# Optimization experiments

Measured on AMD Instinct MI355X. Metric: run time of the kernel, lower is better.

## Reference

```python
import jax, jax.numpy as jnp
from jax import lax
import numpy as np

DIM = 256
QK = 256          # qk_dim defaults to dim
HEADS = 8
NWIN = 7
TOPK = 4
KS = 3            # side_dwconv


def setup_inputs() -> dict:
    key = jax.random.key(0)
    ks = jax.random.split(key, 8)
    B, H, W = 1, 112, 112
    s = lambda d: 1.0 / np.sqrt(d)
    return {
        "x": jax.random.normal(ks[0], (B, H, W, DIM), jnp.float32),
        # fused qkv linear: dim -> qk + qk + dim
        "w_qkv": jax.random.normal(ks[1], (DIM, 2 * QK + DIM), jnp.float32) * s(DIM),
        "b_qkv": jnp.zeros((2 * QK + DIM,), jnp.float32),
        # output projection
        "w_o": jax.random.normal(ks[2], (DIM, DIM), jnp.float32) * s(DIM),
        "b_o": jnp.zeros((DIM,), jnp.float32),
        # depthwise 3x3 lepe conv (HWIO with I=1, groups=dim)
        "lepe_w": jax.random.normal(ks[3], (KS, KS, 1, DIM), jnp.float32) * s(KS * KS),
        "lepe_b": jnp.zeros((DIM,), jnp.float32),
    }


def _win2img(t, B, H, W, c):
    # (B, p2, h, w, c) windows -> (B, H, W, c) image
    hw, ww = H // NWIN, W // NWIN
    t = t.reshape(B, NWIN, NWIN, hw, ww, c)
    return t.transpose(0, 1, 3, 2, 4, 5).reshape(B, H, W, c)


def reference(x, w_qkv, b_qkv, w_o, b_o, lepe_w, lepe_b):
    B, H, W, C = x.shape
    hw, ww = H // NWIN, W // NWIN
    p2, w2 = NWIN * NWIN, hw * ww
    hd_q, hd_v = QK // HEADS, DIM // HEADS
    scale = QK ** (-0.5)

    # partition into windows: (B, p2, hw, ww, C)
    xp = x.reshape(B, NWIN, hw, NWIN, ww, C).transpose(0, 1, 3, 2, 4, 5)
    xp = xp.reshape(B, p2, hw, ww, C)

    qkv = xp @ w_qkv + b_qkv
    q, kv = qkv[..., :QK], qkv[..., QK:]          # (B,p2,hw,ww,QK), (...,QK+DIM)

    q_pix = q.reshape(B, p2, w2, QK)
    kv_pix = kv.reshape(B, p2, w2, QK + DIM)      # identity kv_down

    # region-level routing (detached in original since diff_routing=False)
    q_win = lax.stop_gradient(q.mean((2, 3)))     # (B,p2,QK)
    k_win = lax.stop_gradient(kv[..., :QK].mean((2, 3)))
    logit = (q_win * scale) @ jnp.swapaxes(k_win, -1, -2)   # (B,p2,p2)
    top_logit, top_idx = lax.top_k(logit, TOPK)             # (B,p2,TOPK)
    r_weight = jax.nn.softmax(top_logit, axis=-1)           # unused: mul_weight='none'

    # gather top-k regions' KV: (B, p2, TOPK, w2, QK+DIM)
    kv_sel = jax.vmap(lambda kvb, idxb: kvb[idxb])(kv_pix, top_idx)

    k_sel = kv_sel[..., :QK].reshape(B, p2, TOPK * w2, HEADS, hd_q)
    v_sel = kv_sel[..., QK:].reshape(B, p2, TOPK * w2, HEADS, hd_v)
    qh = q_pix.reshape(B, p2, w2, HEADS, hd_q)

    attn = jnp.einsum('bpqhc,bpkhc->bphqk', qh * scale, k_sel)
    attn = jax.nn.softmax(attn, axis=-1)
    out = jnp.einsum('bphqk,bpkhc->bpqhc', attn, v_sel).reshape(B, p2, hw, ww, DIM)
    out = _win2img(out, B, H, W, DIM)

    # lepe: depthwise conv over v in image layout
    v_img = _win2img(kv[..., QK:], B, H, W, DIM)
    lepe = lax.conv_general_dilated(
        v_img, lepe_w, (1, 1), 'SAME',
        dimension_numbers=('NHWC', 'HWIO', 'NHWC'),
        feature_group_count=DIM) + lepe_b

    return (out + lepe) @ w_o + b_o
```

## Files before the change

### kernel.cpp

```cpp
#include <hip/hip_runtime.h>
#include <math.h>


typedef __bf16 bf16x8 __attribute__((ext_vector_type(8)));
typedef __bf16 bf16x4 __attribute__((ext_vector_type(4)));
typedef float f32x4 __attribute__((ext_vector_type(4)));

__global__ __launch_bounds__(64)
void pack1(const float* __restrict__ w_qkv, const float* __restrict__ w_o,
           __bf16* __restrict__ wtq, __bf16* __restrict__ wto,
           float* __restrict__ qkwin) {
    const int b = blockIdx.x;
    const int t = threadIdx.x;
    if (b < 768) {
        int n = b;
        int k = t * 4;
        bf16x4 o;
        o[0] = (__bf16)w_qkv[(k + 0) * 768 + n];
        o[1] = (__bf16)w_qkv[(k + 1) * 768 + n];
        o[2] = (__bf16)w_qkv[(k + 2) * 768 + n];
        o[3] = (__bf16)w_qkv[(k + 3) * 768 + n];
        *(bf16x4*)(wtq + (size_t)n * 256 + k) = o;
    } else if (b < 1024) {
        int n = b - 768;
        int k = t * 4;
        bf16x4 o;
        o[0] = (__bf16)w_o[(k + 0) * 256 + n];
        o[1] = (__bf16)w_o[(k + 1) * 256 + n];
        o[2] = (__bf16)w_o[(k + 2) * 256 + n];
        o[3] = (__bf16)w_o[(k + 3) * 256 + n];
        *(bf16x4*)(wto + (size_t)n * 256 + k) = o;
    } else {
        int idx = (b - 1024) * 64 + t;
        *(float4*)(qkwin + (size_t)idx * 4) = (float4){0.f, 0.f, 0.f, 0.f};
    }
}

template<int QKV>
__global__ __launch_bounds__(256)
void gemm_bf16(const __bf16* __restrict__ A,
               const float* __restrict__ Ax,
               const __bf16* __restrict__ Wt,
               const float* __restrict__ bias,
               float* __restrict__ C, int N,
               __bf16* __restrict__ Qp,
               __bf16* __restrict__ Kp,
               __bf16* __restrict__ vbf,
               __bf16* __restrict__ Vt,
               float* __restrict__ q_win,
               float* __restrict__ k_win) {
    const int t = threadIdx.x & 63;
    const int wv = threadIdx.x >> 6;
    const int l16 = t & 15, quad = t >> 4;
    const int m0 = blockIdx.x * 64;
    const int n0 = blockIdx.y * 128 + wv * 32;

    __shared__ __bf16 Vs[128][72];

    int mrow[4];
#pragma unroll
    for (int nt = 0; nt < 4; nt++) {
        const int m = m0 + nt * 16 + l16;
        if (QKV == 1) {
            const int p = m >> 8, pix = m & 255;
            mrow[nt] = ((p / 7) * 16 + (pix >> 4)) * 112 + (p % 7) * 16 + (pix & 15);
        } else {
            mrow[nt] = m;
        }
    }

    f32x4 acc[2][4];
#pragma unroll
    for (int km = 0; km < 2; km++)
#pragma unroll
        for (int nt = 0; nt < 4; nt++) acc[km][nt] = (f32x4){0.f, 0.f, 0.f, 0.f};

#pragma unroll
    for (int ks = 0; ks < 8; ks++) {
        bf16x8 Af[2], Bf[4];
#pragma unroll
        for (int km = 0; km < 2; km++)
            Af[km] = *(const bf16x8*)(Wt + (size_t)(n0 + km * 16 + l16) * 256 + ks * 32 + quad * 8);
#pragma unroll
        for (int nt = 0; nt < 4; nt++) {
            if (QKV == 1) {
                const float* s = Ax + (size_t)mrow[nt] * 256 + ks * 32 + quad * 8;
                const float4 f0 = *(const float4*)s;
                const float4 f1 = *(const float4*)(s + 4);
                bf16x8 bv;
                bv[0] = (__bf16)f0.x; bv[1] = (__bf16)f0.y;
                bv[2] = (__bf16)f0.z; bv[3] = (__bf16)f0.w;
                bv[4] = (__bf16)f1.x; bv[5] = (__bf16)f1.y;
                bv[6] = (__bf16)f1.z; bv[7] = (__bf16)f1.w;
                Bf[nt] = bv;
            } else {
                Bf[nt] = *(const bf16x8*)(A + (size_t)mrow[nt] * 256 + ks * 32 + quad * 8);
            }
        }
#pragma unroll
        for (int km = 0; km < 2; km++)
#pragma unroll
            for (int nt = 0; nt < 4; nt++)
                acc[km][nt] = __builtin_amdgcn_mfma_f32_16x16x32_bf16(
                    Af[km], Bf[nt], acc[km][nt], 0, 0, 0);
    }

    float ws[2][4];
#pragma unroll
    for (int km = 0; km < 2; km++)
#pragma unroll
        for (int j = 0; j < 4; j++) ws[km][j] = 0.f;

#pragma unroll
    for (int km = 0; km < 2; km++) {
        const int n = n0 + km * 16 + quad * 4;
        float4 b4 = *(const float4*)(bias + n);
#pragma unroll
        for (int nt = 0; nt < 4; nt++) {
            const int m = m0 + nt * 16 + l16;
            float v0 = acc[km][nt][0] + b4.x;
            float v1 = acc[km][nt][1] + b4.y;
            float v2 = acc[km][nt][2] + b4.z;
            float v3 = acc[km][nt][3] + b4.w;
            if (QKV == 0) {
                float4 o = {v0, v1, v2, v3};
                *(float4*)(C + (size_t)m * N + n) = o;
            } else {
                const int p = m >> 8, pix = m & 255;
                if (n0 < 512) {
                    ws[km][0] += v0; ws[km][1] += v1;
                    ws[km][2] += v2; ws[km][3] += v3;
                }
                if (n0 < 256) {
                    const float s = 1.4426950408889634f / 16.0f;
                    int h = n >> 5, cc = n & 31;
                    bf16x4 o;
                    o[0] = (__bf16)(v0 * s); o[1] = (__bf16)(v1 * s);
                    o[2] = (__bf16)(v2 * s); o[3] = (__bf16)(v3 * s);
                    *(bf16x4*)(Qp + ((size_t)((p * 8 + h) * 256 + pix)) * 32 + cc) = o;
                } else if (n0 < 512) {
                    int n2 = n - 256;
                    int h = n2 >> 5, cc = n2 & 31;
                    bf16x4 o;
                    o[0] = (__bf16)v0; o[1] = (__bf16)v1;
                    o[2] = (__bf16)v2; o[3] = (__bf16)v3;
                    *(bf16x4*)(Kp + ((size_t)((p * 8 + h) * 256 + pix)) * 32 + cc) = o;
                } else {
                    int n2 = n - 512;
                    int imgrow = ((p / 7) * 16 + (pix >> 4)) * 112 + (p % 7) * 16 + (pix & 15);
                    bf16x4 o;
                    o[0] = (__bf16)v0; o[1] = (__bf16)v1;
                    o[2] = (__bf16)v2; o[3] = (__bf16)v3;
                    *(bf16x4*)(vbf + (size_t)imgrow * 256 + n2) = o;
                    const int cbase = wv * 32 + km * 16 + quad * 4;
                    const int pb = nt * 16 + l16;
                    Vs[cbase + 0][pb] = o[0];
                    Vs[cbase + 1][pb] = o[1];
                    Vs[cbase + 2][pb] = o[2];
                    Vs[cbase + 3][pb] = o[3];
                }
            }
        }
    }

    if (QKV == 1 && n0 < 512) {
        const int pblk = m0 >> 8;
#pragma unroll
        for (int km = 0; km < 2; km++) {
#pragma unroll
            for (int j = 0; j < 4; j++) {
                float s = ws[km][j];
                s += __shfl_xor(s, 1);
                s += __shfl_xor(s, 2);
                s += __shfl_xor(s, 4);
                s += __shfl_xor(s, 8);
                ws[km][j] = s;
            }
            if (l16 == 0) {
                const int n = n0 + km * 16 + quad * 4;
                float* dst = (n < 256) ? (q_win + pblk * 256 + n)
                                       : (k_win + pblk * 256 + (n - 256));
                atomicAdd(dst + 0, ws[km][0]);
                atomicAdd(dst + 1, ws[km][1]);
                atomicAdd(dst + 2, ws[km][2]);
                atomicAdd(dst + 3, ws[km][3]);
            }
        }
    }

    if (QKV == 1 && blockIdx.y >= 4) {
        __syncthreads();
        const int p_ = m0 >> 8, qt_ = (m0 >> 6) & 3;
        const int vb = blockIdx.y * 128 - 512;
#pragma unroll
        for (int rep = 0; rep < 4; rep++) {
            int id = rep * 256 + threadIdx.x;
            int row = id >> 3, c8 = (id & 7) * 8;
            int hh = (vb + row) >> 5, c32 = (vb + row) & 31;
            bf16x8 val = *(const bf16x8*)&Vs[row][c8];
            *(bf16x8*)(Vt + ((size_t)((p_ * 8 + hh) * 32 + c32)) * 256 + qt_ * 64 + c8) = val;
        }
    }
}

__global__ __launch_bounds__(64)
void routing_topk(const float* __restrict__ q_win,
                  const float* __restrict__ k_win,
                  int* __restrict__ top_idx) {
    const int r = blockIdx.x;
    const int j = threadIdx.x;
    __shared__ float vals[64];

    float d = -1e30f;
    if (j < 49) {
        const float4* qp = (const float4*)(q_win + r * 256);
        const float4* kp = (const float4*)(k_win + j * 256);
        float s = 0.f;
#pragma unroll
        for (int c = 0; c < 64; c++) {
            float4 a = qp[c], b = kp[c];
            s += a.x * b.x + a.y * b.y + a.z * b.z + a.w * b.w;
        }
        d = s;
    }
    vals[j] = d;
    __syncthreads();
    if (j == 0) {
        float bv0 = -1e30f, bv1 = -1e30f, bv2 = -1e30f, bv3 = -1e30f;
        int bi0 = 0, bi1 = 0, bi2 = 0, bi3 = 0;
        for (int q = 0; q < 49; q++) {
            float v = vals[q];
            if (v > bv0) {
                bv3 = bv2; bi3 = bi2; bv2 = bv1; bi2 = bi1; bv1 = bv0; bi1 = bi0;
                bv0 = v; bi0 = q;
            } else if (v > bv1) {
                bv3 = bv2; bi3 = bi2; bv2 = bv1; bi2 = bi1; bv1 = v; bi1 = q;
            } else if (v > bv2) {
                bv3 = bv2; bi3 = bi2; bv2 = v; bi2 = q;
            } else if (v > bv3) {
                bv3 = v; bi3 = q;
            }
        }
        top_idx[r * 4 + 0] = bi0;
        top_idx[r * 4 + 1] = bi1;
        top_idx[r * 4 + 2] = bi2;
        top_idx[r * 4 + 3] = bi3;
    }
}

#define PLDS_PITCH 68
#define HALO_PITCH 36

__global__ __launch_bounds__(256)
void attn_mfma(const __bf16* __restrict__ Qp,
               const __bf16* __restrict__ Kp,
               const __bf16* __restrict__ Vt,
               const int* __restrict__ top_idx,
               const __bf16* __restrict__ vbf,
               const float* __restrict__ lw,
               const float* __restrict__ lb,
               __bf16* __restrict__ prebf) {
    const int bb = blockIdx.x;
    const int qt = bb / 392;
    const int ph = bb - qt * 392;
    const int p = ph >> 3;
    const int h = ph & 7;
    const int t = threadIdx.x & 63;
    const int wv = threadIdx.x >> 6;
    const int l16 = t & 15, quad = t >> 4;

    __shared__ union {
        unsigned short Plds[4][64 * PLDS_PITCH];
        struct {
            f32x4 O[4][2][4][64];
            float l[4][4][64];
        } red;
    } U;
    __shared__ __bf16 Hs[108 * HALO_PITCH];

    unsigned short* const Pw = U.Plds[wv];

    bf16x8 Qf[4];
#pragma unroll
    for (int nt = 0; nt < 4; nt++)
        Qf[nt] = *(const bf16x8*)(Qp + ((size_t)((p * 8 + h) * 256 + qt * 64 + nt * 16 + l16)) * 32 + quad * 8);

    const int sel = top_idx[p * 4 + wv];
    const __bf16* const Kb = Kp + ((size_t)(sel * 8 + h)) * 8192;
    const __bf16* const Vb = Vt + ((size_t)(sel * 8 + h)) * 8192;

    float lstate[4] = {0.f, 0.f, 0.f, 0.f};
    f32x4 O[2][4];
#pragma unroll
    for (int mt = 0; mt < 2; mt++)
#pragma unroll
        for (int nt = 0; nt < 4; nt++) O[mt][nt] = (f32x4){0.f, 0.f, 0.f, 0.f};

    bf16x8 Kf[4];
#pragma unroll
    for (int km = 0; km < 4; km++)
        Kf[km] = *(const bf16x8*)(Kb + (size_t)(km * 16 + l16) * 32 + quad * 8);

    for (int kc = 0; kc < 4; kc++) {
        const int kbase = kc * 64;

        bf16x8 Vf[2][2];
#pragma unroll
        for (int ks = 0; ks < 2; ks++)
#pragma unroll
            for (int mt = 0; mt < 2; mt++)
                Vf[ks][mt] = *(const bf16x8*)(Vb + (size_t)(mt * 16 + l16) * 256 + kbase + ks * 32 + quad * 8);

        const int kbn = (kc < 3 ? kc + 1 : 3) * 64;
        bf16x8 Kn[4];
#pragma unroll
        for (int km = 0; km < 4; km++)
            Kn[km] = *(const bf16x8*)(Kb + (size_t)(kbn + km * 16 + l16) * 32 + quad * 8);

#pragma unroll
        for (int nt = 0; nt < 4; nt++) {
            f32x4 S[4];
            __builtin_amdgcn_s_setprio(1);
#pragma unroll
            for (int km = 0; km < 4; km++)
                S[km] = __builtin_amdgcn_mfma_f32_16x16x32_bf16(
                    Kf[km], Qf[nt], (f32x4){0.f, 0.f, 0.f, 0.f}, 0, 0, 0);
            __builtin_amdgcn_s_setprio(0);

            float rs = 0.f;
#pragma unroll
            for (int km = 0; km < 4; km++) {
                union { unsigned short u[4]; ushort4 v; } pk;
#pragma unroll
                for (int r = 0; r < 4; r++) {
                    float pv = __builtin_amdgcn_exp2f(S[km][r]);
                    rs += pv;
                    pk.u[r] = __builtin_bit_cast(unsigned short, (__bf16)pv);
                }
                *(ushort4*)&Pw[(nt * 16 + l16) * PLDS_PITCH + km * 16 + quad * 4] = pk.v;
            }
            rs += __shfl_xor(rs, 16);
            rs += __shfl_xor(rs, 32);
            lstate[nt] += rs;
        }

#pragma unroll
        for (int ks = 0; ks < 2; ks++) {
#pragma unroll
            for (int nt = 0; nt < 4; nt++) {
                int idx = (nt * 16 + l16) * PLDS_PITCH + ks * 32 + quad * 8;
                union { ushort4 u4[2]; bf16x8 v; } pu;
                pu.u4[0] = *(const ushort4*)&Pw[idx];
                pu.u4[1] = *(const ushort4*)&Pw[idx + 4];
                __builtin_amdgcn_s_setprio(1);
#pragma unroll
                for (int mt = 0; mt < 2; mt++)
                    O[mt][nt] = __builtin_amdgcn_mfma_f32_16x16x32_bf16(
                        Vf[ks][mt], pu.v, O[mt][nt], 0, 0, 0);
                __builtin_amdgcn_s_setprio(0);
            }
        }

#pragma unroll
        for (int km = 0; km < 4; km++) Kf[km] = Kn[km];
    }

    __syncthreads();
#pragma unroll
    for (int mt = 0; mt < 2; mt++)
#pragma unroll
        for (int nt = 0; nt < 4; nt++)
            U.red.O[wv][mt][nt][t] = O[mt][nt];
#pragma unroll
    for (int nt = 0; nt < 4; nt++)
        U.red.l[wv][nt][t] = lstate[nt];

    const int pr = p / 7, pc = p % 7;
    if (threadIdx.x < 108) {
        const int i = threadIdx.x;
        int hy = i / 18, hx = i - hy * 18;
        int gy = pr * 16 + qt * 4 - 1 + hy;
        int gx = pc * 16 - 1 + hx;
        union { bf16x4 v4[8]; bf16x8 v8[4]; uint4 q[4]; } u;
        u.q[0] = (uint4){0u, 0u, 0u, 0u};
        u.q[1] = (uint4){0u, 0u, 0u, 0u};
        u.q[2] = (uint4){0u, 0u, 0u, 0u};
        u.q[3] = (uint4){0u, 0u, 0u, 0u};
        if (gy >= 0 && gy < 112 && gx >= 0 && gx < 112) {
            const __bf16* src = vbf + ((size_t)(gy * 112 + gx)) * 256 + h * 32;
            u.v8[0] = *(const bf16x8*)src;
            u.v8[1] = *(const bf16x8*)(src + 8);
            u.v8[2] = *(const bf16x8*)(src + 16);
            u.v8[3] = *(const bf16x8*)(src + 24);
        }
#pragma unroll
        for (int j = 0; j < 8; j++)
            *(bf16x4*)&Hs[i * HALO_PITCH + j * 4] = u.v4[j];
    }
    __syncthreads();

    const int nt = wv;
    const float ltot = U.red.l[0][nt][t] + U.red.l[1][nt][t]
                     + U.red.l[2][nt][t] + U.red.l[3][nt][t];
    const float inv = 1.f / ltot;
    const int himg = pr * 16 + qt * 4 + nt, wimg = pc * 16 + l16;
#pragma unroll
    for (int mt = 0; mt < 2; mt++) {
        f32x4 o = U.red.O[0][mt][nt][t];
#pragma unroll
        for (int v = 1; v < 4; v++) {
            f32x4 ov = U.red.O[v][mt][nt][t];
            o[0] += ov[0]; o[1] += ov[1]; o[2] += ov[2]; o[3] += ov[3];
        }
        const int c = h * 32 + mt * 16 + quad * 4;
        const float4 lbv = *(const float4*)(lb + c);
        float a0 = lbv.x, a1 = lbv.y, a2 = lbv.z, a3 = lbv.w;
#pragma unroll
        for (int dh = 0; dh < 3; dh++)
#pragma unroll
            for (int dw = 0; dw < 3; dw++) {
                const float4 w4 = *(const float4*)(lw + (dh * 3 + dw) * 256 + c);
                const bf16x4 v4 = *(const bf16x4*)&Hs[((nt + dh) * 18 + l16 + dw) * HALO_PITCH + mt * 16 + quad * 4];
                a0 += (float)v4[0] * w4.x;
                a1 += (float)v4[1] * w4.y;
                a2 += (float)v4[2] * w4.z;
                a3 += (float)v4[3] * w4.w;
            }
        bf16x4 ob;
        ob[0] = (__bf16)(o[0] * inv + a0);
        ob[1] = (__bf16)(o[1] * inv + a1);
        ob[2] = (__bf16)(o[2] * inv + a2);
        ob[3] = (__bf16)(o[3] * inv + a3);
        *(bf16x4*)(prebf + ((size_t)(himg * 112 + wimg)) * 256 + c) = ob;
    }
}

extern "C" void kernel_launch(void* const* d_in, const int* in_sizes, int n_in,
                              void* d_out, int out_size, void* d_ws, size_t ws_size,
                              hipStream_t stream) {
    const float* x      = (const float*)d_in[0];
    const float* w_qkv  = (const float*)d_in[1];
    const float* b_qkv  = (const float*)d_in[2];
    const float* w_o    = (const float*)d_in[3];
    const float* b_o    = (const float*)d_in[4];
    const float* lepe_w = (const float*)d_in[5];
    const float* lepe_b = (const float*)d_in[6];
    float* out = (float*)d_out;

    char* w = (char*)d_ws;
    __bf16* Qp    = (__bf16*)w; w += 6422528;
    __bf16* Kp    = (__bf16*)w; w += 6422528;
    __bf16* vbf   = (__bf16*)w; w += 6422528;
    __bf16* Vt    = (__bf16*)w; w += 6422528;
    __bf16* prebf = (__bf16*)w; w += 6422528;
    __bf16* wtq   = (__bf16*)w; w += 393216;
    __bf16* wto   = (__bf16*)w; w += 131072;
    float* q_win   = (float*)w; w += 12544 * 4;
    float* k_win   = (float*)w; w += 12544 * 4;
    int*   top_idx = (int*)w;

    pack1<<<768 + 256 + 98, 64, 0, stream>>>(w_qkv, w_o, wtq, wto, q_win);
    gemm_bf16<1><<<dim3(196, 6), 256, 0, stream>>>(nullptr, x, wtq, b_qkv,
                                                   nullptr, 0, Qp, Kp, vbf, Vt,
                                                   q_win, k_win);
    routing_topk<<<49, 64, 0, stream>>>(q_win, k_win, top_idx);
    attn_mfma<<<392 * 4, 256, 0, stream>>>(Qp, Kp, Vt, top_idx,
                                           vbf, lepe_w, lepe_b, prebf);
    gemm_bf16<0><<<dim3(196, 2), 256, 0, stream>>>(prebf, nullptr, wto, b_o,
                                                   out, 256, nullptr, nullptr, nullptr, nullptr,
                                                   nullptr, nullptr);
}
```

Measured before the change: 192.7 us.

## Stage GEMM activation tile in shared memory and prefetch weight fragments

The GEMM kernel now cooperatively loads the 64x256 activation tile into LDS once per block, converting fp32 to bf16 in the QKV case, instead of each wave re-reading and re-converting it from global memory. The LDS buffer is aliased with the existing V-transpose scratch, and a barrier is added before that reuse. Weight fragments are also software-prefetched one k-step ahead. This cuts redundant global traffic and conversion work across the four waves, at the cost of more LDS per block, which may lower occupancy, plus extra barriers.

```diff
diff --git a/kernel.cpp b/kernel.cpp
--- a/kernel.cpp
+++ b/kernel.cpp
@@ -55,19 +55,34 @@
     const int m0 = blockIdx.x * 64;
     const int n0 = blockIdx.y * 128 + wv * 32;
 
-    __shared__ __bf16 Vs[128][72];
-
-    int mrow[4];
-#pragma unroll
-    for (int nt = 0; nt < 4; nt++) {
-        const int m = m0 + nt * 16 + l16;
-        if (QKV == 1) {
-            const int p = m >> 8, pix = m & 255;
-            mrow[nt] = ((p / 7) * 16 + (pix >> 4)) * 112 + (p % 7) * 16 + (pix & 15);
-        } else {
-            mrow[nt] = m;
-        }
-    }
+    __shared__ __align__(16) char smem[33792];
+    __bf16 (*const As)[264] = (__bf16(*)[264])smem;
+    __bf16 (*const Vs)[72]  = (__bf16(*)[72])smem;
+
+    if (QKV == 1) {
+        const int p = m0 >> 8, pixbase = m0 & 255;
+        const int rowbase0 = (p / 7) * 16 * 112 + (p % 7) * 16;
+#pragma unroll
+        for (int it = 0; it < 16; it++) {
+            const int j = it * 1024 + threadIdx.x * 4;
+            const int r = j >> 8, col = j & 255;
+            const int pix = pixbase + r;
+            const int ir = rowbase0 + (pix >> 4) * 112 + (pix & 15);
+            const float4 f = *(const float4*)(Ax + (size_t)ir * 256 + col);
+            bf16x4 o;
+            o[0] = (__bf16)f.x; o[1] = (__bf16)f.y;
+            o[2] = (__bf16)f.z; o[3] = (__bf16)f.w;
+            *(bf16x4*)&As[r][col] = o;
+        }
+    } else {
+#pragma unroll
+        for (int it = 0; it < 8; it++) {
+            const int j = it * 2048 + threadIdx.x * 8;
+            const int r = j >> 8, col = j & 255;
+            *(bf16x8*)&As[r][col] = *(const bf16x8*)(A + (size_t)(m0 + r) * 256 + col);
+        }
+    }
+    __syncthreads();
 
     f32x4 acc[2][4];
 #pragma unroll
@@ -75,35 +90,36 @@
 #pragma unroll
         for (int nt = 0; nt < 4; nt++) acc[km][nt] = (f32x4){0.f, 0.f, 0.f, 0.f};
 
+    bf16x8 Afc[2];
+#pragma unroll
+    for (int km = 0; km < 2; km++)
+        Afc[km] = *(const bf16x8*)(Wt + (size_t)(n0 + km * 16 + l16) * 256 + quad * 8);
+
 #pragma unroll
     for (int ks = 0; ks < 8; ks++) {
-        bf16x8 Af[2], Bf[4];
+        bf16x8 Afn[2];
+        const int ksn = (ks < 7) ? ks + 1 : 7;
 #pragma unroll
         for (int km = 0; km < 2; km++)
-            Af[km] = *(const bf16x8*)(Wt + (size_t)(n0 + km * 16 + l16) * 256 + ks * 32 + quad * 8);
-#pragma unroll
-        for (int nt = 0; nt < 4; nt++) {
-            if (QKV == 1) {
-                const float* s = Ax + (size_t)mrow[nt] * 256 + ks * 32 + quad * 8;
-                const float4 f0 = *(const float4*)s;
-                const float4 f1 = *(const float4*)(s + 4);
-                bf16x8 bv;
-                bv[0] = (__bf16)f0.x; bv[1] = (__bf16)f0.y;
-                bv[2] = (__bf16)f0.z; bv[3] = (__bf16)f0.w;
-                bv[4] = (__bf16)f1.x; bv[5] = (__bf16)f1.y;
-                bv[6] = (__bf16)f1.z; bv[7] = (__bf16)f1.w;
-                Bf[nt] = bv;
-            } else {
-                Bf[nt] = *(const bf16x8*)(A + (size_t)mrow[nt] * 256 + ks * 32 + quad * 8);
-            }
-        }
+            Afn[km] = *(const bf16x8*)(Wt + (size_t)(n0 + km * 16 + l16) * 256 + ksn * 32 + quad * 8);
+
+        bf16x8 Bf[4];
+#pragma unroll
+        for (int nt = 0; nt < 4; nt++)
+            Bf[nt] = *(const bf16x8*)&As[nt * 16 + l16][ks * 32 + quad * 8];
+
 #pragma unroll
         for (int km = 0; km < 2; km++)
 #pragma unroll
             for (int nt = 0; nt < 4; nt++)
                 acc[km][nt] = __builtin_amdgcn_mfma_f32_16x16x32_bf16(
-                    Af[km], Bf[nt], acc[km][nt], 0, 0, 0);
-    }
+                    Afc[km], Bf[nt], acc[km][nt], 0, 0, 0);
+
+#pragma unroll
+        for (int km = 0; km < 2; km++) Afc[km] = Afn[km];
+    }
+
+    if (QKV == 1 && blockIdx.y >= 4) __syncthreads();
 
     float ws[2][4];
 #pragma unroll
```

Measured after the change: 157.9 us. 1.22x faster.
